# Performance work log

Hardware: AMD Instinct MI355X
Metric: run time of the kernel (lower is better)

## Reference

```python
import jax, jax.numpy as jnp
import numpy as np

N, E, H, C = 10000, 160000, 2, 512  # nodes, edges, GAT heads, per-head channels


def _add_self_loops(src, dst, n):
    loop = jnp.arange(n, dtype=src.dtype)
    return jnp.concatenate([src, loop]), jnp.concatenate([dst, loop])


def _gcn(x, W, b, src, dst, n):
    # PyG GCNConv: add self-loops, symmetric deg^-1/2 normalization, scatter-add to dst.
    s, d = _add_self_loops(src, dst, n)
    h = x @ W
    deg = jax.ops.segment_sum(jnp.ones(s.shape[0], h.dtype), d, num_segments=n)
    dinv = jnp.where(deg > 0, jax.lax.rsqrt(deg), 0.0)
    norm = dinv[s] * dinv[d]                    # [E+N]
    out = jax.ops.segment_sum(h[s] * norm[:, None], d, num_segments=n)
    return out + b


def _gat(x, W, a_src, a_dst, b, src, dst, n):
    # PyG GATConv (heads=2, concat=True): per-edge LeakyReLU(0.2) scores,
    # segment softmax over incoming edges of each dst node, weighted scatter-add.
    s, d = _add_self_loops(src, dst, n)
    h = (x @ W).reshape(n, H, C)                # [N,H,C]
    al_s = jnp.einsum('nhc,hc->nh', h, a_src)   # [N,H]
    al_d = jnp.einsum('nhc,hc->nh', h, a_dst)
    e = jax.nn.leaky_relu(al_s[s] + al_d[d], 0.2)          # [E+N,H]
    emax = jax.ops.segment_max(e, d, num_segments=n)
    emax = jnp.where(jnp.isfinite(emax), emax, 0.0)
    ex = jnp.exp(e - emax[d])
    esum = jax.ops.segment_sum(ex, d, num_segments=n)
    alpha = ex / (esum[d] + 1e-16)                          # [E+N,H]
    out = jax.ops.segment_sum(h[s] * alpha[:, :, None], d, num_segments=n)
    return out.reshape(n, H * C) + b


def _pdist(x):
    # torch.cdist(x, x, p=2) with zero-safe sqrt (grad 0 on diagonal).
    sq = jnp.sum(x * x, axis=-1)
    d2 = jnp.maximum(sq[:, None] + sq[None, :] - 2.0 * (x @ x.T), 0.0)
    safe = jnp.where(d2 > 0, d2, 1.0)
    return jnp.where(d2 > 0, jnp.sqrt(safe), 0.0)


def setup_inputs() -> dict:
    key = jax.random.key(0)
    ks = jax.random.split(key, 16)
    w = lambda k, s, fan: (jax.random.normal(k, s, jnp.float32) / np.sqrt(fan)).astype(jnp.float32)
    z = lambda s: jnp.zeros(s, jnp.float32)
    x = jax.random.normal(ks[0], (N, 512), jnp.float32)
    edge_index = jax.random.randint(ks[1], (2, E), 0, N, dtype=jnp.int32)
    return {
        'x': x, 'edge_index': edge_index,
        'enc_gat_W': w(ks[2], (512, H * C), 512), 'enc_gat_asrc': w(ks[3], (H, C), C),
        'enc_gat_adst': w(ks[4], (H, C), C), 'enc_gat_b': z(H * C),
        'enc_gcn_W': w(ks[5], (1024, 512), 1024), 'enc_gcn_b': z(512),
        'densea_W': w(ks[6], (512, 128), 512), 'densea_b': z(128),
        'latent_W': w(ks[7], (128, 64), 128), 'latent_b': z(64),
        'dec1_W': w(ks[8], (64, 128), 64), 'dec1_b': z(128),
        'dec2_W': w(ks[9], (128, 512), 128), 'dec2_b': z(512),
        'dec_gcn_W': w(ks[10], (512, 512), 512), 'dec_gcn_b': z(512),
        'dec_gat_W': w(ks[11], (512, H * C), 512), 'dec_gat_asrc': w(ks[12], (H, C), C),
        'dec_gat_adst': w(ks[13], (H, C), C), 'dec_gat_b': z(H * C),
    }


def reference(x, edge_index,
              enc_gat_W, enc_gat_asrc, enc_gat_adst, enc_gat_b,
              enc_gcn_W, enc_gcn_b, densea_W, densea_b, latent_W, latent_b,
              dec1_W, dec1_b, dec2_W, dec2_b, dec_gcn_W, dec_gcn_b,
              dec_gat_W, dec_gat_asrc, dec_gat_adst, dec_gat_b):
    # Dropout layers act as identity in eval mode.
    src, dst = edge_index[0], edge_index[1]
    n = x.shape[0]
    # Encoder
    h = jax.nn.relu(_gat(x, enc_gat_W, enc_gat_asrc, enc_gat_adst, enc_gat_b, src, dst, n))
    h = jax.nn.relu(_gcn(h, enc_gcn_W, enc_gcn_b, src, dst, n))
    h = jax.nn.relu(h @ densea_W + densea_b)
    z = h @ latent_W + latent_b
    # Decoder
    d = jax.nn.relu(z @ dec1_W + dec1_b)
    d = jax.nn.relu(d @ dec2_W + dec2_b)
    d = jax.nn.relu(_gcn(d, dec_gcn_W, dec_gcn_b, src, dst, n))
    d = _gat(d, dec_gat_W, dec_gat_asrc, dec_gat_adst, dec_gat_b, src, dst, n)
    return _pdist(d)
```

## Files before the change

### kernel.cpp

```cpp
#include <hip/hip_runtime.h>
#include <math.h>

#define NNODES 10000
#define NEDGES 160000
#define EN_TOT (NNODES + NEDGES)
#define NBLK 79
#define NTRI 3160

typedef __attribute__((ext_vector_type(8))) short bf16x8;
typedef __attribute__((ext_vector_type(4))) float f32x4;
typedef __attribute__((address_space(1))) const void g_void;
typedef __attribute__((address_space(3))) void l_void;

static __device__ __forceinline__ unsigned enc_f(float f) {
    unsigned b = __float_as_uint(f);
    return (b & 0x80000000u) ? ~b : (b | 0x80000000u);
}
static __device__ __forceinline__ float dec_f(unsigned u) {
    unsigned b = (u & 0x80000000u) ? (u & 0x7FFFFFFFu) : ~u;
    return __uint_as_float(b);
}
static __device__ __forceinline__ unsigned short f2bf(float f) {
    unsigned u = __float_as_uint(f);
    return (unsigned short)((u + 0x7FFFu + ((u >> 16) & 1u)) >> 16);
}

__global__ __launch_bounds__(256) void gemm64(
    const float* __restrict__ A, const float* __restrict__ B,
    const float* __restrict__ bias, float* __restrict__ C,
    int M, int K, int Nn, int act) {
    __shared__ float As[16][68];
    __shared__ float Bs[16][68];
    int tid = threadIdx.x;
    int tx = tid & 15, ty = tid >> 4;
    int row0 = blockIdx.y * 64, col0 = blockIdx.x * 64;
    float acc[4][4] = {};
    for (int k0 = 0; k0 < K; k0 += 16) {
        int r = tid >> 2, c4 = (tid & 3) << 2;
        float4 av = make_float4(0.f, 0.f, 0.f, 0.f);
        if (row0 + r < M) av = *(const float4*)&A[(size_t)(row0 + r) * K + k0 + c4];
        As[c4 + 0][r] = av.x; As[c4 + 1][r] = av.y; As[c4 + 2][r] = av.z; As[c4 + 3][r] = av.w;
        int kk = tid >> 4, n4 = (tid & 15) << 2;
        *(float4*)&Bs[kk][n4] = *(const float4*)&B[(size_t)(k0 + kk) * Nn + col0 + n4];
        __syncthreads();
#pragma unroll
        for (int k2 = 0; k2 < 16; k2++) {
            float4 a4 = *(float4*)&As[k2][ty * 4];
            float4 b4 = *(float4*)&Bs[k2][tx * 4];
            float aa[4] = {a4.x, a4.y, a4.z, a4.w};
            float bb[4] = {b4.x, b4.y, b4.z, b4.w};
#pragma unroll
            for (int i = 0; i < 4; i++)
#pragma unroll
                for (int j = 0; j < 4; j++) acc[i][j] += aa[i] * bb[j];
        }
        __syncthreads();
    }
#pragma unroll
    for (int i = 0; i < 4; i++) {
        int gm = row0 + ty * 4 + i;
        if (gm >= M) continue;
        float4 v;
        float* vp = &v.x;
#pragma unroll
        for (int j = 0; j < 4; j++) {
            float t = acc[i][j];
            if (bias) t += bias[col0 + tx * 4 + j];
            if (act) t = fmaxf(t, 0.f);
            vp[j] = t;
        }
        *(float4*)&C[(size_t)gm * Nn + col0 + tx * 4] = v;
    }
}

__global__ __launch_bounds__(128) void gat_scores(
    const float* __restrict__ h, const float* __restrict__ a_src,
    const float* __restrict__ a_dst, float* __restrict__ als, float* __restrict__ ald) {
    int n = blockIdx.x;
    int w = threadIdx.x >> 6;
    int l = threadIdx.x & 63;
    const float* hp = h + (size_t)n * 1024 + w * 512 + l * 8;
    const float* asp = a_src + w * 512 + l * 8;
    const float* adp = a_dst + w * 512 + l * 8;
    float s = 0.f, d = 0.f;
#pragma unroll
    for (int i = 0; i < 8; i++) { float hv = hp[i]; s += hv * asp[i]; d += hv * adp[i]; }
#pragma unroll
    for (int off = 32; off; off >>= 1) { s += __shfl_down(s, off); d += __shfl_down(d, off); }
    if (l == 0) { als[n * 2 + w] = s; ald[n * 2 + w] = d; }
}

__global__ void k_count(const int* __restrict__ ei, int* __restrict__ cnt) {
    int e = blockIdx.x * blockDim.x + threadIdx.x;
    if (e >= EN_TOT) return;
    int d = (e < NEDGES) ? ei[NEDGES + e] : (e - NEDGES);
    atomicAdd(&cnt[d], 1);
}

__global__ __launch_bounds__(256) void k_scan(
    const int* __restrict__ cnt, int* __restrict__ rowstart,
    int* __restrict__ cursor, float* __restrict__ dinv) {
    __shared__ int buf[256];
    __shared__ int carry;
    int t = threadIdx.x;
    if (t == 0) carry = 0;
    __syncthreads();
    for (int base = 0; base < NNODES; base += 256) {
        int i = base + t;
        int v = (i < NNODES) ? cnt[i] : 0;
        buf[t] = v;
        __syncthreads();
        for (int off = 1; off < 256; off <<= 1) {
            int x = (t >= off) ? buf[t - off] : 0;
            __syncthreads();
            buf[t] += x;
            __syncthreads();
        }
        int incl = buf[t];
        int cbase = carry;
        if (i < NNODES) {
            int rs = cbase + incl - v;
            rowstart[i] = rs;
            cursor[i] = rs;
            dinv[i] = (v > 0) ? rsqrtf((float)v) : 0.f;
        }
        __syncthreads();
        if (t == 255) carry = cbase + incl;
        __syncthreads();
    }
    if (t == 0) rowstart[NNODES] = carry;
}

__global__ void k_fill(const int* __restrict__ ei, int* __restrict__ cursor,
                       int* __restrict__ csr_src, int* __restrict__ csr_eid) {
    int e = blockIdx.x * blockDim.x + threadIdx.x;
    if (e >= EN_TOT) return;
    int s, d;
    if (e < NEDGES) { s = ei[e]; d = ei[NEDGES + e]; } else { s = e - NEDGES; d = s; }
    int pos = atomicAdd(&cursor[d], 1);
    csr_src[pos] = s;
    csr_eid[pos] = e;
}

__global__ void k_init_gat(unsigned* __restrict__ emax, float* __restrict__ esum) {
    int i = blockIdx.x * blockDim.x + threadIdx.x;
    if (i < NNODES * 2) { emax[i] = 0x007FFFFFu; esum[i] = 0.f; }
}

__global__ void k_edge_score(const int* __restrict__ ei, const float* __restrict__ als,
                             const float* __restrict__ ald, float* __restrict__ score,
                             unsigned* __restrict__ emax) {
    int e = blockIdx.x * blockDim.x + threadIdx.x;
    if (e >= EN_TOT) return;
    int s, d;
    if (e < NEDGES) { s = ei[e]; d = ei[NEDGES + e]; } else { s = e - NEDGES; d = s; }
#pragma unroll
    for (int h = 0; h < 2; h++) {
        float v = als[s * 2 + h] + ald[d * 2 + h];
        v = (v > 0.f) ? v : 0.2f * v;
        score[e * 2 + h] = v;
        atomicMax(&emax[d * 2 + h], enc_f(v));
    }
}

__global__ void k_edge_exp(const int* __restrict__ ei, float* __restrict__ score,
                           const unsigned* __restrict__ emax, float* __restrict__ esum) {
    int e = blockIdx.x * blockDim.x + threadIdx.x;
    if (e >= EN_TOT) return;
    int d = (e < NEDGES) ? ei[NEDGES + e] : (e - NEDGES);
#pragma unroll
    for (int h = 0; h < 2; h++) {
        float m = dec_f(emax[d * 2 + h]);
        float x = expf(score[e * 2 + h] - m);
        score[e * 2 + h] = x;
        atomicAdd(&esum[d * 2 + h], x);
    }
}

__global__ __launch_bounds__(256) void gat_aggregate(
    const float* __restrict__ hfeat, const float* __restrict__ ex,
    const float* __restrict__ esum, const int* __restrict__ rowstart,
    const int* __restrict__ csr_src, const int* __restrict__ csr_eid,
    const float* __restrict__ bias, float* __restrict__ out, int act) {
    int n = blockIdx.x;
    int t = threadIdx.x;
    int c0 = t * 4;
    int head = c0 >> 9;
    float inv = 1.f / (esum[n * 2 + head] + 1e-16f);
    int beg = rowstart[n], end = rowstart[n + 1];
    float4 acc = make_float4(0.f, 0.f, 0.f, 0.f);
    for (int p = beg; p < end; p++) {
        int s = csr_src[p];
        int eid = csr_eid[p];
        float alpha = ex[eid * 2 + head] * inv;
        float4 hv = *(const float4*)&hfeat[(size_t)s * 1024 + c0];
        acc.x += alpha * hv.x; acc.y += alpha * hv.y;
        acc.z += alpha * hv.z; acc.w += alpha * hv.w;
    }
    float4 bv = *(const float4*)&bias[c0];
    acc.x += bv.x; acc.y += bv.y; acc.z += bv.z; acc.w += bv.w;
    if (act) {
        acc.x = fmaxf(acc.x, 0.f); acc.y = fmaxf(acc.y, 0.f);
        acc.z = fmaxf(acc.z, 0.f); acc.w = fmaxf(acc.w, 0.f);
    }
    *(float4*)&out[(size_t)n * 1024 + c0] = acc;
}

__global__ __launch_bounds__(128) void gcn_aggregate(
    const float* __restrict__ hfeat, const float* __restrict__ dinv,
    const int* __restrict__ rowstart, const int* __restrict__ csr_src,
    const float* __restrict__ bias, float* __restrict__ out, int act) {
    int n = blockIdx.x;
    int t = threadIdx.x;
    int c0 = t * 4;
    float dn = dinv[n];
    int beg = rowstart[n], end = rowstart[n + 1];
    float4 acc = make_float4(0.f, 0.f, 0.f, 0.f);
    for (int p = beg; p < end; p++) {
        int s = csr_src[p];
        float w = dinv[s] * dn;
        float4 hv = *(const float4*)&hfeat[(size_t)s * 512 + c0];
        acc.x += w * hv.x; acc.y += w * hv.y; acc.z += w * hv.z; acc.w += w * hv.w;
    }
    float4 bv = *(const float4*)&bias[c0];
    acc.x += bv.x; acc.y += bv.y; acc.z += bv.z; acc.w += bv.w;
    if (act) {
        acc.x = fmaxf(acc.x, 0.f); acc.y = fmaxf(acc.y, 0.f);
        acc.z = fmaxf(acc.z, 0.f); acc.w = fmaxf(acc.w, 0.f);
    }
    *(float4*)&out[(size_t)n * 512 + c0] = acc;
}

__global__ __launch_bounds__(256) void k_split_blk(
    const float* __restrict__ X, unsigned short* __restrict__ Ghi,
    unsigned short* __restrict__ Glo) {
    __shared__ float T[128][69];
    const int nb = blockIdx.y;
    const int ct = blockIdx.x;
    const int t = threadIdx.x;
#pragma unroll
    for (int it = 0; it < 8; it++) {
        int idx = it * 256 + t;
        int r = idx >> 4;
        int c4 = (idx & 15) << 2;
        int node = nb * 128 + r;
        float4 v = make_float4(0.f, 0.f, 0.f, 0.f);
        if (node < NNODES) v = *(const float4*)&X[(size_t)node * 1024 + ct * 64 + c4];
        T[r][c4 + 0] = v.x; T[r][c4 + 1] = v.y; T[r][c4 + 2] = v.z; T[r][c4 + 3] = v.w;
    }
    __syncthreads();
#pragma unroll
    for (int it = 0; it < 4; it++) {
        int idx = it * 256 + t;
        int kcl = idx >> 7;
        int r = idx & 127;
        int kc = ct * 8 + kcl;
        size_t go = (((size_t)nb * 128 + kc) * 128 + r) * 8;
        unsigned hv[4], lv[4];
#pragma unroll
        for (int p = 0; p < 4; p++) {
            float f0 = T[r][kcl * 8 + 2 * p];
            float f1 = T[r][kcl * 8 + 2 * p + 1];
            unsigned short h0 = f2bf(f0), h1 = f2bf(f1);
            unsigned short l0 = f2bf(f0 - __uint_as_float((unsigned)h0 << 16));
            unsigned short l1 = f2bf(f1 - __uint_as_float((unsigned)h1 << 16));
            hv[p] = (unsigned)h0 | ((unsigned)h1 << 16);
            lv[p] = (unsigned)l0 | ((unsigned)l1 << 16);
        }
        *(uint4*)&Ghi[go] = make_uint4(hv[0], hv[1], hv[2], hv[3]);
        *(uint4*)&Glo[go] = make_uint4(lv[0], lv[1], lv[2], lv[3]);
    }
}

__global__ __launch_bounds__(256) void k_sqn(const float* __restrict__ X,
                                             float* __restrict__ sqn) {
    __shared__ float wsum[4];
    int n = blockIdx.x;
    int t = threadIdx.x;
    float4 v = *(const float4*)&X[(size_t)n * 1024 + t * 4];
    float s = v.x * v.x + v.y * v.y + v.z * v.z + v.w * v.w;
#pragma unroll
    for (int off = 32; off; off >>= 1) s += __shfl_down(s, off);
    if ((t & 63) == 0) wsum[t >> 6] = s;
    __syncthreads();
    if (t == 0) sqn[n] = wsum[0] + wsum[1] + wsum[2] + wsum[3];
}

__global__ __launch_bounds__(256) void k_gram_pdist(
    const unsigned short* __restrict__ Ghi, const unsigned short* __restrict__ Glo,
    const float* __restrict__ sq, float* __restrict__ out) {
    __shared__ unsigned short lds[16384];
    const int tid = threadIdx.x;
    const int lane = tid & 63;
    const int w = tid >> 6;

    int bid = blockIdx.x;
    int u = (bid & 7) * (NTRI / 8) + (bid >> 3);
    int bi = (int)((double)NBLK + 0.5 - sqrt(((double)NBLK + 0.5) * ((double)NBLK + 0.5) - 2.0 * (double)u));
    if (bi < 0) bi = 0;
    if (bi > NBLK - 1) bi = NBLK - 1;
    auto cum = [](int r) { return r * NBLK - (r * (r - 1)) / 2; };
    while (bi + 1 <= NBLK - 1 && cum(bi + 1) <= u) bi++;
    while (bi > 0 && cum(bi) > u) bi--;
    const int bj = bi + (u - cum(bi));
    const int row0 = bi * 128;
    const int col0 = bj * 128;
    const int wr = w >> 1, wc = w & 1;

    const unsigned short* mat = (w & 1) ? Glo : Ghi;
    const int nbq = (w < 2) ? bi : bj;
    const unsigned short* base = mat + (size_t)nbq * 131072;

    f32x4 acc[4][4];
#pragma unroll
    for (int i = 0; i < 4; i++)
#pragma unroll
        for (int j = 0; j < 4; j++) acc[i][j] = (f32x4){0.f, 0.f, 0.f, 0.f};

    const int q = lane >> 4;
    const int r16 = lane & 15;

    for (int kc0 = 0; kc0 < 128; kc0 += 4) {
        const unsigned short* gp0 = base + (size_t)kc0 * 1024;
#pragma unroll
        for (int s = 0; s < 8; s++) {
            const unsigned short* gp = gp0 + s * 512 + lane * 8;
            unsigned short* lp = &lds[w * 4096 + s * 512];
            __builtin_amdgcn_global_load_lds((g_void*)gp, (l_void*)lp, 16, 0, 0);
        }
        __syncthreads();

        bf16x8 ah[4], al[4], bh[4], bl[4];
#pragma unroll
        for (int t = 0; t < 4; t++) {
            int aoff = q * 1024 + (wr * 64 + t * 16 + r16) * 8;
            ah[t] = *(const bf16x8*)&lds[aoff];
            al[t] = *(const bf16x8*)&lds[4096 + aoff];
            int boff = q * 1024 + (wc * 64 + t * 16 + r16) * 8;
            bh[t] = *(const bf16x8*)&lds[8192 + boff];
            bl[t] = *(const bf16x8*)&lds[12288 + boff];
        }
#pragma unroll
        for (int i = 0; i < 4; i++)
#pragma unroll
            for (int j = 0; j < 4; j++) {
                acc[i][j] = __builtin_amdgcn_mfma_f32_16x16x32_bf16(ah[i], bh[j], acc[i][j], 0, 0, 0);
                acc[i][j] = __builtin_amdgcn_mfma_f32_16x16x32_bf16(ah[i], bl[j], acc[i][j], 0, 0, 0);
                acc[i][j] = __builtin_amdgcn_mfma_f32_16x16x32_bf16(al[i], bh[j], acc[i][j], 0, 0, 0);
            }
        __syncthreads();
    }

    const int q4 = (lane >> 4) << 2;
    float sqj[4];
    int gj[4];
#pragma unroll
    for (int j = 0; j < 4; j++) {
        gj[j] = col0 + wc * 64 + j * 16 + r16;
        sqj[j] = (gj[j] < NNODES) ? sq[gj[j]] : 0.f;
    }
#pragma unroll
    for (int i = 0; i < 4; i++) {
        int gibase = row0 + wr * 64 + i * 16 + q4;
        bool iv = gibase < NNODES;
        float4 sqi = iv ? *(const float4*)&sq[gibase] : make_float4(0.f, 0.f, 0.f, 0.f);
        float* sqip = &sqi.x;
#pragma unroll
        for (int j = 0; j < 4; j++) {
            if (!iv || gj[j] >= NNODES) continue;
            float dv[4];
#pragma unroll
            for (int r = 0; r < 4; r++) {
                float d2 = sqip[r] + sqj[j] - 2.f * acc[i][j][r];
                float d = sqrtf(fmaxf(d2, 0.f));
                if (gibase + r == gj[j]) d = 0.f;
                dv[r] = d;
            }
#pragma unroll
            for (int r = 0; r < 4; r++)
                __builtin_nontemporal_store(dv[r], &out[(size_t)(gibase + r) * NNODES + gj[j]]);
            f32x4 mv = {dv[0], dv[1], dv[2], dv[3]};
            __builtin_nontemporal_store(mv, (f32x4*)&out[(size_t)gj[j] * NNODES + gibase]);
        }
    }
}

extern "C" void kernel_launch(void* const* d_in, const int* in_sizes, int n_in,
                              void* d_out, int out_size, void* d_ws, size_t ws_size,
                              hipStream_t stream) {
    const float* x            = (const float*)d_in[0];
    const int*   ei           = (const int*)d_in[1];
    const float* enc_gat_W    = (const float*)d_in[2];
    const float* enc_gat_asrc = (const float*)d_in[3];
    const float* enc_gat_adst = (const float*)d_in[4];
    const float* enc_gat_b    = (const float*)d_in[5];
    const float* enc_gcn_W    = (const float*)d_in[6];
    const float* enc_gcn_b    = (const float*)d_in[7];
    const float* densea_W     = (const float*)d_in[8];
    const float* densea_b     = (const float*)d_in[9];
    const float* latent_W     = (const float*)d_in[10];
    const float* latent_b     = (const float*)d_in[11];
    const float* dec1_W       = (const float*)d_in[12];
    const float* dec1_b       = (const float*)d_in[13];
    const float* dec2_W       = (const float*)d_in[14];
    const float* dec2_b       = (const float*)d_in[15];
    const float* dec_gcn_W    = (const float*)d_in[16];
    const float* dec_gcn_b    = (const float*)d_in[17];
    const float* dec_gat_W    = (const float*)d_in[18];
    const float* dec_gat_asrc = (const float*)d_in[19];
    const float* dec_gat_adst = (const float*)d_in[20];
    const float* dec_gat_b    = (const float*)d_in[21];

    float* out = (float*)d_out;

    const size_t GSZ = (size_t)NBLK * 131072;
    unsigned short* Xhi = (unsigned short*)d_ws;
    unsigned short* Xlo = Xhi + GSZ;
    float*    sqn      = (float*)(Xlo + GSZ);
    float*    score    = sqn + 10000;
    float*    esum     = score + 340000;
    unsigned* emax     = (unsigned*)(esum + 20000);
    float*    als      = (float*)(emax + 20000);
    float*    ald      = als + 20000;
    int*      cnt      = (int*)(ald + 20000);
    int*      cursor   = cnt + 10000;
    int*      rowstart = cursor + 10000;
    float*    dinv     = (float*)(rowstart + 10001);
    int*      csr_src  = (int*)(dinv + 10000);
    int*      csr_eid  = csr_src + 170000;

    float* bufA = out;
    float* bufB = out + 10500000;
    float* bufC = out + 21000000;
    float* bufD = out + 26500000;
    float* h128 = out + 32000000;
    float* z64  = out + 33500000;
    float* d128 = out + 34500000;

    const int NT = 256;
    dim3 eb((EN_TOT + NT - 1) / NT);

    hipMemsetAsync(cnt, 0, NNODES * sizeof(int), stream);
    k_count<<<eb, NT, 0, stream>>>(ei, cnt);
    k_scan<<<1, 256, 0, stream>>>(cnt, rowstart, cursor, dinv);
    k_fill<<<eb, NT, 0, stream>>>(ei, cursor, csr_src, csr_eid);

    auto gemm = [&](const float* A, const float* W, const float* bias, float* Cc,
                    int M, int K, int Nn, int act) {
        dim3 g(Nn / 64, (M + 63) / 64);
        gemm64<<<g, 256, 0, stream>>>(A, W, bias, Cc, M, K, Nn, act);
    };

    gemm(x, enc_gat_W, nullptr, bufA, NNODES, 512, 1024, 0);
    gat_scores<<<NNODES, 128, 0, stream>>>(bufA, enc_gat_asrc, enc_gat_adst, als, ald);
    k_init_gat<<<(2 * NNODES + 255) / 256, 256, 0, stream>>>(emax, esum);
    k_edge_score<<<eb, NT, 0, stream>>>(ei, als, ald, score, emax);
    k_edge_exp<<<eb, NT, 0, stream>>>(ei, score, emax, esum);
    gat_aggregate<<<NNODES, 256, 0, stream>>>(bufA, score, esum, rowstart, csr_src,
                                              csr_eid, enc_gat_b, bufB, 1);

    gemm(bufB, enc_gcn_W, nullptr, bufC, NNODES, 1024, 512, 0);
    gcn_aggregate<<<NNODES, 128, 0, stream>>>(bufC, dinv, rowstart, csr_src,
                                              enc_gcn_b, bufD, 1);

    gemm(bufD, densea_W, densea_b, h128, NNODES, 512, 128, 1);
    gemm(h128, latent_W, latent_b, z64, NNODES, 128, 64, 0);
    gemm(z64, dec1_W, dec1_b, d128, NNODES, 64, 128, 1);
    gemm(d128, dec2_W, dec2_b, bufC, NNODES, 128, 512, 1);

    gemm(bufC, dec_gcn_W, nullptr, bufD, NNODES, 512, 512, 0);
    gcn_aggregate<<<NNODES, 128, 0, stream>>>(bufD, dinv, rowstart, csr_src,
                                              dec_gcn_b, bufC, 1);

    gemm(bufC, dec_gat_W, nullptr, bufA, NNODES, 512, 1024, 0);
    gat_scores<<<NNODES, 128, 0, stream>>>(bufA, dec_gat_asrc, dec_gat_adst, als, ald);
    k_init_gat<<<(2 * NNODES + 255) / 256, 256, 0, stream>>>(emax, esum);
    k_edge_score<<<eb, NT, 0, stream>>>(ei, als, ald, score, emax);
    k_edge_exp<<<eb, NT, 0, stream>>>(ei, score, emax, esum);
    gat_aggregate<<<NNODES, 256, 0, stream>>>(bufA, score, esum, rowstart, csr_src,
                                              csr_eid, dec_gat_b, bufB, 0);

    dim3 sg(16, NBLK);
    k_split_blk<<<sg, 256, 0, stream>>>(bufB, Xhi, Xlo);
    k_sqn<<<NNODES, 256, 0, stream>>>(bufB, sqn);
    k_gram_pdist<<<NTRI, 256, 0, stream>>>(Xhi, Xlo, sqn, out);
}
```

Before: 1.781 ms.

## Route large dense GEMMs through split-bf16 MFMA kernel with pre-blocked operands

Adds a weight split kernel and a 128x128-tile MFMA GEMM that takes bf16 hi/lo operand pairs (three MFMAs per tile product) and generalizes the activation split kernel to any K. The large layer GEMMs now split activations and weights into blocked bf16 layouts and run on matrix cores instead of the previous fp32 gemm64 path. The aim is to cut FP32 GEMM time at roughly fp32-level accuracy, at the cost of extra split kernels and memory traffic per GEMM.

```diff
diff --git a/kernel.cpp b/kernel.cpp
--- a/kernel.cpp
+++ b/kernel.cpp
@@ -233,11 +233,12 @@
 
 __global__ __launch_bounds__(256) void k_split_blk(
     const float* __restrict__ X, unsigned short* __restrict__ Ghi,
-    unsigned short* __restrict__ Glo) {
+    unsigned short* __restrict__ Glo, int K) {
     __shared__ float T[128][69];
     const int nb = blockIdx.y;
     const int ct = blockIdx.x;
     const int t = threadIdx.x;
+    const int KC = K >> 3;
 #pragma unroll
     for (int it = 0; it < 8; it++) {
         int idx = it * 256 + t;
@@ -245,7 +246,7 @@
         int c4 = (idx & 15) << 2;
         int node = nb * 128 + r;
         float4 v = make_float4(0.f, 0.f, 0.f, 0.f);
-        if (node < NNODES) v = *(const float4*)&X[(size_t)node * 1024 + ct * 64 + c4];
+        if (node < NNODES) v = *(const float4*)&X[(size_t)node * K + ct * 64 + c4];
         T[r][c4 + 0] = v.x; T[r][c4 + 1] = v.y; T[r][c4 + 2] = v.z; T[r][c4 + 3] = v.w;
     }
     __syncthreads();
@@ -255,7 +256,7 @@
         int kcl = idx >> 7;
         int r = idx & 127;
         int kc = ct * 8 + kcl;
-        size_t go = (((size_t)nb * 128 + kc) * 128 + r) * 8;
+        size_t go = (((size_t)nb * KC + kc) * 128 + r) * 8;
         unsigned hv[4], lv[4];
 #pragma unroll
         for (int p = 0; p < 4; p++) {
@@ -269,6 +270,112 @@
         }
         *(uint4*)&Ghi[go] = make_uint4(hv[0], hv[1], hv[2], hv[3]);
         *(uint4*)&Glo[go] = make_uint4(lv[0], lv[1], lv[2], lv[3]);
+    }
+}
+
+__global__ __launch_bounds__(256) void k_splitw(
+    const float* __restrict__ W, unsigned short* __restrict__ Whi,
+    unsigned short* __restrict__ Wlo, int K, int N) {
+    const int cb = blockIdx.y;
+    const int t = threadIdx.x;
+    const int c = t & 127;
+    const int kc = blockIdx.x * 2 + (t >> 7);
+    const int col = cb * 128 + c;
+    const int KC = K >> 3;
+    unsigned hv[4], lv[4];
+#pragma unroll
+    for (int p = 0; p < 4; p++) {
+        float f0 = W[(size_t)(kc * 8 + 2 * p) * N + col];
+        float f1 = W[(size_t)(kc * 8 + 2 * p + 1) * N + col];
+        unsigned short h0 = f2bf(f0), h1 = f2bf(f1);
+        unsigned short l0 = f2bf(f0 - __uint_as_float((unsigned)h0 << 16));
+        unsigned short l1 = f2bf(f1 - __uint_as_float((unsigned)h1 << 16));
+        hv[p] = (unsigned)h0 | ((unsigned)h1 << 16);
+        lv[p] = (unsigned)l0 | ((unsigned)l1 << 16);
+    }
+    size_t go = (((size_t)cb * KC + kc) * 128 + c) * 8;
+    *(uint4*)&Whi[go] = make_uint4(hv[0], hv[1], hv[2], hv[3]);
+    *(uint4*)&Wlo[go] = make_uint4(lv[0], lv[1], lv[2], lv[3]);
+}
+
+__global__ __launch_bounds__(256) void gemm_mfma(
+    const unsigned short* __restrict__ AHi, const unsigned short* __restrict__ ALo,
+    const unsigned short* __restrict__ BHi, const unsigned short* __restrict__ BLo,
+    const float* __restrict__ bias, float* __restrict__ C,
+    int KC, int N, int act) {
+    __shared__ unsigned short lds[16384];
+    const int tid = threadIdx.x;
+    const int lane = tid & 63;
+    const int w = tid >> 6;
+    const int bi = blockIdx.y;
+    const int bj = blockIdx.x;
+    const int wr = w >> 1, wc = w & 1;
+
+    const unsigned short* mat = (w < 2) ? ((w & 1) ? ALo : AHi) : ((w & 1) ? BLo : BHi);
+    const int nbq = (w < 2) ? bi : bj;
+    const unsigned short* base = mat + (size_t)nbq * KC * 1024;
+
+    f32x4 acc[4][4];
+#pragma unroll
+    for (int i = 0; i < 4; i++)
+#pragma unroll
+        for (int j = 0; j < 4; j++) acc[i][j] = (f32x4){0.f, 0.f, 0.f, 0.f};
+
+    const int q = lane >> 4;
+    const int r16 = lane & 15;
+
+    for (int kc0 = 0; kc0 < KC; kc0 += 4) {
+        const unsigned short* gp0 = base + (size_t)kc0 * 1024;
+#pragma unroll
+        for (int s = 0; s < 8; s++) {
+            const unsigned short* gp = gp0 + s * 512 + lane * 8;
+            unsigned short* lp = &lds[w * 4096 + s * 512];
+            __builtin_amdgcn_global_load_lds((g_void*)gp, (l_void*)lp, 16, 0, 0);
+        }
+        __syncthreads();
+
+        bf16x8 ah[4], al[4], bh[4], bl[4];
+#pragma unroll
+        for (int t = 0; t < 4; t++) {
+            int aoff = q * 1024 + (wr * 64 + t * 16 + r16) * 8;
+            ah[t] = *(const bf16x8*)&lds[aoff];
+            al[t] = *(const bf16x8*)&lds[4096 + aoff];
+            int boff = q * 1024 + (wc * 64 + t * 16 + r16) * 8;
+            bh[t] = *(const bf16x8*)&lds[8192 + boff];
+            bl[t] = *(const bf16x8*)&lds[12288 + boff];
+        }
+#pragma unroll
+        for (int i = 0; i < 4; i++)
+#pragma unroll
+            for (int j = 0; j < 4; j++) {
+                acc[i][j] = __builtin_amdgcn_mfma_f32_16x16x32_bf16(ah[i], bh[j], acc[i][j], 0, 0, 0);
+                acc[i][j] = __builtin_amdgcn_mfma_f32_16x16x32_bf16(ah[i], bl[j], acc[i][j], 0, 0, 0);
+                acc[i][j] = __builtin_amdgcn_mfma_f32_16x16x32_bf16(al[i], bh[j], acc[i][j], 0, 0, 0);
+            }
+        __syncthreads();
+    }
+
+    const int q4 = (lane >> 4) << 2;
+    float bv[4];
+    int gj[4];
+#pragma unroll
+    for (int j = 0; j < 4; j++) {
+        gj[j] = bj * 128 + wc * 64 + j * 16 + r16;
+        bv[j] = bias ? bias[gj[j]] : 0.f;
+    }
+#pragma unroll
+    for (int i = 0; i < 4; i++) {
+        int gibase = bi * 128 + wr * 64 + i * 16 + q4;
+        if (gibase >= NNODES) continue;
+#pragma unroll
+        for (int j = 0; j < 4; j++) {
+#pragma unroll
+            for (int r = 0; r < 4; r++) {
+                float t = acc[i][j][r] + bv[j];
+                if (act) t = fmaxf(t, 0.f);
+                C[(size_t)(gibase + r) * N + gj[j]] = t;
+            }
+        }
     }
 }
 
@@ -428,6 +535,8 @@
     float*    dinv     = (float*)(rowstart + 10001);
     int*      csr_src  = (int*)(dinv + 10000);
     int*      csr_eid  = csr_src + 170000;
+    unsigned short* WtHi = (unsigned short*)(csr_eid + 170000);
+    unsigned short* WtLo = WtHi + 524288;
 
     float* bufA = out;
     float* bufB = out + 10500000;
@@ -450,8 +559,18 @@
         dim3 g(Nn / 64, (M + 63) / 64);
         gemm64<<<g, 256, 0, stream>>>(A, W, bias, Cc, M, K, Nn, act);
     };
-
-    gemm(x, enc_gat_W, nullptr, bufA, NNODES, 512, 1024, 0);
+    auto mgemm = [&](const float* A, const float* W, const float* bias, float* Cc,
+                     int K, int Nn, int act) {
+        int KC = K >> 3;
+        dim3 sg(K / 64, NBLK);
+        k_split_blk<<<sg, 256, 0, stream>>>(A, Xhi, Xlo, K);
+        dim3 wg(KC / 2, Nn / 128);
+        k_splitw<<<wg, 256, 0, stream>>>(W, WtHi, WtLo, K, Nn);
+        dim3 gg(Nn / 128, NBLK);
+        gemm_mfma<<<gg, 256, 0, stream>>>(Xhi, Xlo, WtHi, WtLo, bias, Cc, KC, Nn, act);
+    };
+
+    mgemm(x, enc_gat_W, nullptr, bufA, 512, 1024, 0);
     gat_scores<<<NNODES, 128, 0, stream>>>(bufA, enc_gat_asrc, enc_gat_adst, als, ald);
     k_init_gat<<<(2 * NNODES + 255) / 256, 256, 0, stream>>>(emax, esum);
     k_edge_score<<<eb, NT, 0, stream>>>(ei, als, ald, score, emax);
@@ -459,20 +578,20 @@
     gat_aggregate<<<NNODES, 256, 0, stream>>>(bufA, score, esum, rowstart, csr_src,
                                               csr_eid, enc_gat_b, bufB, 1);
 
-    gemm(bufB, enc_gcn_W, nullptr, bufC, NNODES, 1024, 512, 0);
+    mgemm(bufB, enc_gcn_W, nullptr, bufC, 1024, 512, 0);
     gcn_aggregate<<<NNODES, 128, 0, stream>>>(bufC, dinv, rowstart, csr_src,
                                               enc_gcn_b, bufD, 1);
 
-    gemm(bufD, densea_W, densea_b, h128, NNODES, 512, 128, 1);
+    mgemm(bufD, densea_W, densea_b, h128, 512, 128, 1);
     gemm(h128, latent_W, latent_b, z64, NNODES, 128, 64, 0);
     gemm(z64, dec1_W, dec1_b, d128, NNODES, 64, 128, 1);
-    gemm(d128, dec2_W, dec2_b, bufC, NNODES, 128, 512, 1);
-
-    gemm(bufC, dec_gcn_W, nullptr, bufD, NNODES, 512, 512, 0);
+    mgemm(d128, dec2_W, dec2_b, bufC, 128, 512, 1);
+
+    mgemm(bufC, dec_gcn_W, nullptr, bufD, 512, 512, 0);
     gcn_aggregate<<<NNODES, 128, 0, stream>>>(bufD, dinv, rowstart, csr_src,
                                               dec_gcn_b, bufC, 1);
 
-    gemm(bufC, dec_gat_W, nullptr, bufA, NNODES, 512, 1024, 0);
+    mgemm(bufC, dec_gat_W, nullptr, bufA, 512, 1024, 0);
     gat_scores<<<NNODES, 128, 0, stream>>>(bufA, dec_gat_asrc, dec_gat_adst, als, ald);
     k_init_gat<<<(2 * NNODES + 255) / 256, 256, 0, stream>>>(emax, esum);
     k_edge_score<<<eb, NT, 0, stream>>>(ei, als, ald, score, emax);
@@ -481,7 +600,7 @@
                                               csr_eid, dec_gat_b, bufB, 0);
 
     dim3 sg(16, NBLK);
-    k_split_blk<<<sg, 256, 0, stream>>>(bufB, Xhi, Xlo);
+    k_split_blk<<<sg, 256, 0, stream>>>(bufB, Xhi, Xlo, 1024);
     k_sqn<<<NNODES, 256, 0, stream>>>(bufB, sqn);
     k_gram_pdist<<<NTRI, 256, 0, stream>>>(Xhi, Xlo, sqn, out);
 }
```

Result: faster. 1.460 ms (-18.0%).
